# Kernel optimization log

Measured on AMD Instinct MI355X. Metric: run time of the kernel, lower is better.

Reference implementation:

```python
import jax, jax.numpy as jnp
import numpy as np

K = 3
STRIDE = 2
SQRT_D = 4  # in_d_capsules = 16 -> 4x4 matrix pose
LN_EPS = 1e-5


def _unfold(x, k, s):
    # x: [B, N, H, W, A] -> [B, N, k, k, Hout, Wout, A] (matches torch unfold+permute)
    B, N, H, W, A = x.shape
    Hout = (H - k) // s + 1
    Wout = (W - k) // s + 1
    hi = jnp.arange(Hout) * s
    wi = jnp.arange(Wout) * s
    x1 = x[:, :, hi[:, None] + jnp.arange(k)[None, :]]            # [B,N,Hout,k,W,A]
    x2 = x1[:, :, :, :, wi[:, None] + jnp.arange(k)[None, :]]     # [B,N,Hout,k,Wout,k,A]
    return jnp.transpose(x2, (0, 1, 3, 5, 2, 4, 6))               # [B,N,k,k,Hout,Wout,A]


def setup_inputs() -> dict:
    key = jax.random.key(0)
    k1, k2, k3 = jax.random.split(key, 3)
    B, N_in, H, W, D_in = 32, 32, 32, 32, 16
    N_out, D_out = 32, 16
    Hout = (H - K) // STRIDE + 1
    Wout = (W - K) // STRIDE + 1
    w_const = np.sqrt(N_out / (SQRT_D * N_in * K * K)).astype(np.float32)
    return {
        "input": jax.random.normal(k1, (B, N_in, H, W, D_in), dtype=jnp.float32),
        "next_capsule_value": jax.random.normal(k2, (B, N_out, Hout, Wout, D_out), dtype=jnp.float32),
        "w": w_const * jax.random.normal(k3, (K, K, N_in, SQRT_D, SQRT_D, N_out), dtype=jnp.float32),
        "gamma": jnp.ones((D_out,), dtype=jnp.float32),
        "beta": jnp.zeros((D_out,), dtype=jnp.float32),
        "num_iter": 1,
    }


def reference(input, next_capsule_value, w, gamma, beta, num_iter):
    out_d = SQRT_D * SQRT_D
    scale = 1.0 / np.sqrt(out_d).astype(np.float32)
    inp = _unfold(input, K, STRIDE)                                # [B,N,k,k,h,w,A]
    B, N, _, _, h, wd, A = inp.shape
    _inp = inp.reshape(B, N, K, K, h, wd, SQRT_D, SQRT_D)          # bnklhwax
    M = next_capsule_value.shape[1]
    ncv = next_capsule_value.reshape(B, M, h, wd, SQRT_D, SQRT_D)  # bmhwad
    # query-key routing logits
    qk = jnp.einsum('bnklhwax,klnxdm,bmhwad->bnklmhw', _inp, w, ncv) * scale
    qk = jax.nn.softmax(qk, axis=4)
    qk = qk / (jnp.sum(qk, axis=4, keepdims=True) + 1e-10)
    # value aggregation
    out = jnp.einsum('bnklmhw,bnklhwax,klnxdm->bmhwad', qk, _inp, w)
    out = out.reshape(B, M, h, wd, out_d)
    # dropout p=0 -> identity; LayerNorm over capsule dim
    mu = jnp.mean(out, axis=-1, keepdims=True)
    var = jnp.var(out, axis=-1, keepdims=True)
    out = (out - mu) / jnp.sqrt(var + LN_EPS) * gamma + beta
    return out
```

## Files before the change

kernel.cpp:

```cpp
#include <hip/hip_runtime.h>

#define HOUT 15
#define WOUT 15

#define ASG __attribute__((address_space(1)))
#define ASL __attribute__((address_space(3)))

__global__ __launch_bounds__(256, 2) void caps_fused(
    const float* __restrict__ input,
    const float* __restrict__ ncv,
    const float* __restrict__ wt,
    const float* __restrict__ gamma,
    const float* __restrict__ beta,
    float* __restrict__ out)
{
    __shared__ float lw[2][4608];

    const int tid   = threadIdx.x;
    const int grp   = tid >> 5;
    const int lane  = tid & 31;
    const int wv    = tid >> 6;
    const int wlane = tid & 63;

    const int pos = blockIdx.x * 8 + grp;
    const int b   = pos / (HOUT * WOUT);
    const int hw  = pos % (HOUT * WOUT);
    const int h   = hw / WOUT;
    const int wo  = hw % WOUT;

    auto stage = [&](int n, int buf) {
        for (int t = wv; t < 18; t += 4) {
            const int c = t >> 1, half = t & 1;
            const float* src = wt + c * 16384 + n * 512 + half * 256 + wlane * 4;
            float* dst = &lw[buf][c * 512 + half * 256];
            __builtin_amdgcn_global_load_lds((const ASG void*)src, (ASL void*)dst,
                                             16, 0, 0);
        }
    };

    stage(0, 0);

    const float* ncv_p = ncv + ((((size_t)b * 32 + lane) * HOUT + h) * WOUT + wo) * 16;
    float cv[16];
#pragma unroll
    for (int j = 0; j < 16; j += 4) {
        float4 t = *(const float4*)(ncv_p + j);
        cv[j] = t.x; cv[j + 1] = t.y; cv[j + 2] = t.z; cv[j + 3] = t.w;
    }

    float acc[16];
#pragma unroll
    for (int j = 0; j < 16; ++j) acc[j] = 0.0f;

    const int h0 = h * 2, w0 = wo * 2;

    __syncthreads();

    for (int n = 0; n < 32; ++n) {
        if (n + 1 < 32) stage(n + 1, (n + 1) & 1);

        const float* wbuf = lw[n & 1];
        const float* ipn  = input + ((((size_t)b * 32 + n) * 32 + h0) * 32 + w0) * 16;

#pragma unroll
        for (int k = 0; k < 3; ++k) {
#pragma unroll
            for (int l = 0; l < 3; ++l) {
                const int kl = k * 3 + l;
                const float* ip = ipn + (k * 32 + l) * 16;
                float av[16];
#pragma unroll
                for (int j = 0; j < 16; j += 4) {
                    float4 t = *(const float4*)(ip + j);
                    av[j] = t.x; av[j + 1] = t.y; av[j + 2] = t.z; av[j + 3] = t.w;
                }

                const float* wp = wbuf + kl * 512 + lane;

                float u[16];
#pragma unroll
                for (int j = 0; j < 16; ++j) u[j] = 0.0f;
#pragma unroll
                for (int x = 0; x < 4; ++x) {
#pragma unroll
                    for (int d = 0; d < 4; ++d) {
                        float wxd = wp[(x * 4 + d) * 32];
#pragma unroll
                        for (int a = 0; a < 4; ++a)
                            u[a * 4 + d] = fmaf(av[a * 4 + x], wxd, u[a * 4 + d]);
                    }
                }

                float l0 = 0.f, l1 = 0.f, l2 = 0.f, l3 = 0.f;
#pragma unroll
                for (int j = 0; j < 4; ++j) {
                    l0 = fmaf(u[j],      cv[j],      l0);
                    l1 = fmaf(u[j + 4],  cv[j + 4],  l1);
                    l2 = fmaf(u[j + 8],  cv[j + 8],  l2);
                    l3 = fmaf(u[j + 12], cv[j + 12], l3);
                }
                float logit = ((l0 + l1) + (l2 + l3)) * 0.25f;

                float e = __expf(logit);
                float s = e;
#pragma unroll
                for (int o = 16; o > 0; o >>= 1)
                    s += __shfl_xor(s, o, 32);
                float p = e * __builtin_amdgcn_rcpf(s);

#pragma unroll
                for (int j = 0; j < 16; ++j) acc[j] = fmaf(p, u[j], acc[j]);
            }
        }

        if (n < 31) __syncthreads();
    }

    float mu = 0.0f;
#pragma unroll
    for (int j = 0; j < 16; ++j) mu += acc[j];
    mu *= 0.0625f;
    float var = 0.0f;
#pragma unroll
    for (int j = 0; j < 16; ++j) { float d = acc[j] - mu; var = fmaf(d, d, var); }
    var *= 0.0625f;
    float rstd = __builtin_amdgcn_rsqf(var + 1e-5f);

    float* op = out + ((((size_t)b * 32 + lane) * HOUT + h) * WOUT + wo) * 16;
#pragma unroll
    for (int j = 0; j < 16; j += 4) {
        float4 g  = *(const float4*)(gamma + j);
        float4 be = *(const float4*)(beta + j);
        float4 r;
        r.x = (acc[j + 0] - mu) * rstd * g.x + be.x;
        r.y = (acc[j + 1] - mu) * rstd * g.y + be.y;
        r.z = (acc[j + 2] - mu) * rstd * g.z + be.z;
        r.w = (acc[j + 3] - mu) * rstd * g.w + be.w;
        *(float4*)(op + j) = r;
    }
}

extern "C" void kernel_launch(void* const* d_in, const int* in_sizes, int n_in,
                              void* d_out, int out_size, void* d_ws, size_t ws_size,
                              hipStream_t stream) {
    const float* input = (const float*)d_in[0];
    const float* ncv   = (const float*)d_in[1];
    const float* wt    = (const float*)d_in[2];
    const float* gamma = (const float*)d_in[3];
    const float* beta  = (const float*)d_in[4];
    float* out = (float*)d_out;

    caps_fused<<<dim3(900), dim3(256), 0, stream>>>(input, ncv, wt, gamma, beta, out);
}
```

Baseline: 395.3 us.

## Split input-capsule loop across two blocks and use packed v2 FMAs

The n loop over input capsules is split in two along a second grid dimension. Each half writes its partial sums to the output buffer or to workspace, and a separate kernel adds the halves and applies LayerNorm. This doubles the block count from 900 so more of the GPU can be occupied. The inner FMA math is also rewritten with 2-wide float vectors so the compiler can emit packed FMA instructions. The cost is a second launch plus an extra global round trip for the partial results.

New measurement: 377.5 us. 4.5% less time.

```diff
diff --git a/kernel.cpp b/kernel.cpp
--- a/kernel.cpp
+++ b/kernel.cpp
@@ -6,13 +6,14 @@
 #define ASG __attribute__((address_space(1)))
 #define ASL __attribute__((address_space(3)))
 
-__global__ __launch_bounds__(256, 2) void caps_fused(
+typedef float v2 __attribute__((ext_vector_type(2)));
+
+__global__ __launch_bounds__(256, 2) void caps_part(
     const float* __restrict__ input,
     const float* __restrict__ ncv,
     const float* __restrict__ wt,
-    const float* __restrict__ gamma,
-    const float* __restrict__ beta,
-    float* __restrict__ out)
+    float* __restrict__ part0,
+    float* __restrict__ part1)
 {
     __shared__ float lw[2][4608];
 
@@ -28,6 +29,9 @@
     const int h   = hw / WOUT;
     const int wo  = hw % WOUT;
 
+    const int s  = blockIdx.y;
+    const int n0 = s * 16;
+
     auto stage = [&](int n, int buf) {
         for (int t = wv; t < 18; t += 4) {
             const int c = t >> 1, half = t & 1;
@@ -38,28 +42,26 @@
         }
     };
 
-    stage(0, 0);
+    stage(n0, 0);
 
     const float* ncv_p = ncv + ((((size_t)b * 32 + lane) * HOUT + h) * WOUT + wo) * 16;
-    float cv[16];
+    v2 cv2[8];
 #pragma unroll
-    for (int j = 0; j < 16; j += 4) {
-        float4 t = *(const float4*)(ncv_p + j);
-        cv[j] = t.x; cv[j + 1] = t.y; cv[j + 2] = t.z; cv[j + 3] = t.w;
-    }
+    for (int j = 0; j < 8; ++j) cv2[j] = *(const v2*)(ncv_p + j * 2);
 
-    float acc[16];
+    v2 acc2[8];
 #pragma unroll
-    for (int j = 0; j < 16; ++j) acc[j] = 0.0f;
+    for (int j = 0; j < 8; ++j) acc2[j] = (v2){0.0f, 0.0f};
 
     const int h0 = h * 2, w0 = wo * 2;
 
     __syncthreads();
 
-    for (int n = 0; n < 32; ++n) {
-        if (n + 1 < 32) stage(n + 1, (n + 1) & 1);
+    for (int i = 0; i < 16; ++i) {
+        const int n = n0 + i;
+        if (i + 1 < 16) stage(n + 1, (i + 1) & 1);
 
-        const float* wbuf = lw[n & 1];
+        const float* wbuf = lw[i & 1];
         const float* ipn  = input + ((((size_t)b * 32 + n) * 32 + h0) * 32 + w0) * 16;
 
 #pragma unroll
@@ -77,65 +79,100 @@
 
                 const float* wp = wbuf + kl * 512 + lane;
 
-                float u[16];
+                v2 u2[8];
 #pragma unroll
-                for (int j = 0; j < 16; ++j) u[j] = 0.0f;
+                for (int j = 0; j < 8; ++j) u2[j] = (v2){0.0f, 0.0f};
 #pragma unroll
                 for (int x = 0; x < 4; ++x) {
+                    float wd0 = wp[(x * 4 + 0) * 32];
+                    float wd1 = wp[(x * 4 + 1) * 32];
+                    float wd2 = wp[(x * 4 + 2) * 32];
+                    float wd3 = wp[(x * 4 + 3) * 32];
+                    v2 wlo = {wd0, wd1};
+                    v2 whi = {wd2, wd3};
 #pragma unroll
-                    for (int d = 0; d < 4; ++d) {
-                        float wxd = wp[(x * 4 + d) * 32];
-#pragma unroll
-                        for (int a = 0; a < 4; ++a)
-                            u[a * 4 + d] = fmaf(av[a * 4 + x], wxd, u[a * 4 + d]);
+                    for (int a = 0; a < 4; ++a) {
+                        v2 sp = {av[a * 4 + x], av[a * 4 + x]};
+                        u2[a * 2 + 0] = __builtin_elementwise_fma(sp, wlo, u2[a * 2 + 0]);
+                        u2[a * 2 + 1] = __builtin_elementwise_fma(sp, whi, u2[a * 2 + 1]);
                     }
                 }
 
-                float l0 = 0.f, l1 = 0.f, l2 = 0.f, l3 = 0.f;
+                v2 d0 = {0.f, 0.f}, d1 = {0.f, 0.f};
 #pragma unroll
                 for (int j = 0; j < 4; ++j) {
-                    l0 = fmaf(u[j],      cv[j],      l0);
-                    l1 = fmaf(u[j + 4],  cv[j + 4],  l1);
-                    l2 = fmaf(u[j + 8],  cv[j + 8],  l2);
-                    l3 = fmaf(u[j + 12], cv[j + 12], l3);
+                    d0 = __builtin_elementwise_fma(u2[j],     cv2[j],     d0);
+                    d1 = __builtin_elementwise_fma(u2[j + 4], cv2[j + 4], d1);
                 }
-                float logit = ((l0 + l1) + (l2 + l3)) * 0.25f;
+                v2 dd = d0 + d1;
+                float logit = (dd.x + dd.y) * 0.25f;
 
                 float e = __expf(logit);
-                float s = e;
+                float sum = e;
 #pragma unroll
                 for (int o = 16; o > 0; o >>= 1)
-                    s += __shfl_xor(s, o, 32);
-                float p = e * __builtin_amdgcn_rcpf(s);
+                    sum += __shfl_xor(sum, o, 32);
+                float p = e * __builtin_amdgcn_rcpf(sum);
+                v2 p2 = {p, p};
 
 #pragma unroll
-                for (int j = 0; j < 16; ++j) acc[j] = fmaf(p, u[j], acc[j]);
+                for (int j = 0; j < 8; ++j)
+                    acc2[j] = __builtin_elementwise_fma(p2, u2[j], acc2[j]);
             }
         }
 
-        if (n < 31) __syncthreads();
+        if (i < 15) __syncthreads();
+    }
+
+    float* op = (s == 0 ? part0 : part1)
+              + ((((size_t)b * 32 + lane) * HOUT + h) * WOUT + wo) * 16;
+#pragma unroll
+    for (int j = 0; j < 4; ++j) {
+        float4 r;
+        r.x = acc2[2 * j].x;     r.y = acc2[2 * j].y;
+        r.z = acc2[2 * j + 1].x; r.w = acc2[2 * j + 1].y;
+        *(float4*)(op + j * 4) = r;
+    }
+}
+
+__global__ __launch_bounds__(256) void caps_ln(
+    const float* __restrict__ part1,
+    const float* __restrict__ gamma,
+    const float* __restrict__ beta,
+    float* __restrict__ out)
+{
+    const size_t t = (size_t)blockIdx.x * 256 + threadIdx.x;
+    const float* p0 = out   + t * 16;
+    const float* p1 = part1 + t * 16;
+
+    float a[16];
+#pragma unroll
+    for (int j = 0; j < 16; j += 4) {
+        float4 x = *(const float4*)(p0 + j);
+        float4 y = *(const float4*)(p1 + j);
+        a[j] = x.x + y.x; a[j+1] = x.y + y.y; a[j+2] = x.z + y.z; a[j+3] = x.w + y.w;
     }
 
     float mu = 0.0f;
 #pragma unroll
-    for (int j = 0; j < 16; ++j) mu += acc[j];
+    for (int j = 0; j < 16; ++j) mu += a[j];
     mu *= 0.0625f;
     float var = 0.0f;
 #pragma unroll
-    for (int j = 0; j < 16; ++j) { float d = acc[j] - mu; var = fmaf(d, d, var); }
+    for (int j = 0; j < 16; ++j) { float d = a[j] - mu; var = fmaf(d, d, var); }
     var *= 0.0625f;
     float rstd = __builtin_amdgcn_rsqf(var + 1e-5f);
 
-    float* op = out + ((((size_t)b * 32 + lane) * HOUT + h) * WOUT + wo) * 16;
+    float* op = out + t * 16;
 #pragma unroll
     for (int j = 0; j < 16; j += 4) {
         float4 g  = *(const float4*)(gamma + j);
         float4 be = *(const float4*)(beta + j);
         float4 r;
-        r.x = (acc[j + 0] - mu) * rstd * g.x + be.x;
-        r.y = (acc[j + 1] - mu) * rstd * g.y + be.y;
-        r.z = (acc[j + 2] - mu) * rstd * g.z + be.z;
-        r.w = (acc[j + 3] - mu) * rstd * g.w + be.w;
+        r.x = (a[j + 0] - mu) * rstd * g.x + be.x;
+        r.y = (a[j + 1] - mu) * rstd * g.y + be.y;
+        r.z = (a[j + 2] - mu) * rstd * g.z + be.z;
+        r.w = (a[j + 3] - mu) * rstd * g.w + be.w;
         *(float4*)(op + j) = r;
     }
 }
@@ -148,7 +185,9 @@
     const float* wt    = (const float*)d_in[2];
     const float* gamma = (const float*)d_in[3];
     const float* beta  = (const float*)d_in[4];
-    float* out = (float*)d_out;
+    float* out  = (float*)d_out;
+    float* ws   = (float*)d_ws;
 
-    caps_fused<<<dim3(900), dim3(256), 0, stream>>>(input, ncv, wt, gamma, beta, out);
+    caps_part<<<dim3(900, 2), dim3(256), 0, stream>>>(input, ncv, wt, out, ws);
+    caps_ln<<<dim3(900), dim3(256), 0, stream>>>(ws, gamma, beta, out);
 }
```
